# Kernel tuning notes

Measured on AMD Instinct MI355X. Metric: run time of the kernel, lower is better.

Reference implementation:

```python
import math
import jax, jax.numpy as jnp
import numpy as np

B, S, D, H, L, V = 2, 1024, 1024, 16, 6, 256
HD = D // H  # 64
PAD = 0


def setup_inputs() -> dict:
    key = jax.random.key(0)
    ks = jax.random.split(key, 22)
    s = 0.02
    f32 = jnp.float32
    inp = {
        "x": jax.random.randint(ks[0], (B, S), 0, V, dtype=jnp.int32),
        "emb": (jax.random.normal(ks[1], (V, D)) * s).astype(f32),
        "Wq": (jax.random.normal(ks[2], (L, D, D)) * s).astype(f32),
        "bq": jnp.zeros((L, D), f32),
        "Wk": (jax.random.normal(ks[3], (L, D, D)) * s).astype(f32),
        "bk": jnp.zeros((L, D), f32),
        "Wv": (jax.random.normal(ks[4], (L, D, D)) * s).astype(f32),
        "bv": jnp.zeros((L, D), f32),
        "Wo": (jax.random.normal(ks[5], (L, D, D)) * s).astype(f32),
        "bo": jnp.zeros((L, D), f32),
        "W1": (jax.random.normal(ks[6], (L, D, D // 2)) * s).astype(f32),
        "b1": jnp.zeros((L, D // 2), f32),
        "W2": (jax.random.normal(ks[7], (L, D // 2, D)) * s).astype(f32),
        "b2": jnp.zeros((L, D), f32),
        "g1": jnp.ones((L, D), f32),
        "be1": jnp.zeros((L, D), f32),
        "g2": jnp.ones((L, D), f32),
        "be2": jnp.zeros((L, D), f32),
        "E": jax.random.normal(ks[8], (L, S, HD)).astype(f32),  # relative pos embeddings, non-trainable
        "Wf": (jax.random.normal(ks[9], (D, V)) * s).astype(f32),
        "bf": jnp.zeros((V,), f32),
    }
    return inp


def _layernorm(x, g, b, eps=1e-6):
    mu = jnp.mean(x, axis=-1, keepdims=True)
    var = jnp.mean((x - mu) ** 2, axis=-1, keepdims=True)
    return (x - mu) * jax.lax.rsqrt(var + eps) * g + b


def _pos_encoding():
    # embed[p, i] = sin(p * exp(-ln(1e4)*i/D) * exp(ln(1e4)*(i%2)/D) + 0.5*pi*(i%2))
    i = jnp.arange(D, dtype=jnp.float32)
    par = jnp.mod(i, 2.0)
    rate = jnp.exp(-math.log(10000.0) * i / D) * jnp.exp(math.log(10000.0) * par / D)
    pos = jnp.arange(S, dtype=jnp.float32)
    return jnp.sin(pos[:, None] * rate[None, :] + 0.5 * math.pi * par[None, :])  # [S, D]


def _skew(QE):
    # Music Transformer skewing: pad one col on the left, reshape, drop first row.
    padded = jnp.pad(QE, ((0, 0), (0, 0), (0, 0), (1, 0)))  # [B,H,S,S+1]
    reshaped = padded.reshape(B, H, S + 1, S)
    return reshaped[:, :, 1:, :]  # [B,H,S,S]


def reference(x, emb, Wq, bq, Wk, bk, Wv, bv, Wo, bo, W1, b1, W2, b2,
              g1, be1, g2, be2, E, Wf, bf):
    pe = _pos_encoding()
    # look-ahead mask: pad positions OR strictly-future positions
    pad_mask = (x == PAD)[:, None, None, :]                      # [B,1,1,S]
    causal = jnp.triu(jnp.ones((S, S), bool), k=1)[None, None]   # [1,1,S,S]
    neg = (pad_mask | causal).astype(jnp.float32) * -1e9         # [B,1,S,S]
    # QE mask: keep qe[i, j] only where j >= S-1-i (upper-right triangle)
    idx = jnp.arange(S)
    qe_mask = (idx[None, :] >= (S - 1 - idx)[:, None]).astype(jnp.float32)

    h = emb[x] * math.sqrt(D) + pe[None]  # [B,S,D]
    scale = 1.0 / math.sqrt(HD)
    for l in range(L):
        q = (h @ Wq[l] + bq[l]).reshape(B, S, H, HD).transpose(0, 2, 1, 3)
        k = (h @ Wk[l] + bk[l]).reshape(B, S, H, HD).transpose(0, 2, 1, 3)
        v = (h @ Wv[l] + bv[l]).reshape(B, S, H, HD).transpose(0, 2, 1, 3)
        QE = jnp.einsum('bhld,md->bhlm', q, E[l]) * qe_mask
        Srel = _skew(QE)
        logits = (jnp.einsum('bhld,bhmd->bhlm', q, k) + Srel) * scale + neg
        aw = jax.nn.softmax(logits, axis=-1)
        attn = jnp.einsum('bhlm,bhmd->bhld', aw, v)
        attn = attn.transpose(0, 2, 1, 3).reshape(B, S, D)
        ao = attn @ Wo[l] + bo[l]
        o1 = _layernorm(ao, g1[l], be1[l])          # NOTE: no residual, as in source
        f = jax.nn.relu(o1 @ W1[l] + b1[l]) @ W2[l] + b2[l]
        h = _layernorm(f, g2[l], be2[l])
    return h @ Wf + bf  # [B,S,V]
```

## Files before the change

### kernel.cpp

```cpp
#include <hip/hip_runtime.h>
#include <hip/hip_bf16.h>


typedef __attribute__((ext_vector_type(8))) short  s8_t;
typedef __attribute__((ext_vector_type(4))) short  s4_t;
typedef __attribute__((ext_vector_type(8))) __bf16 bf8_t;
typedef __attribute__((ext_vector_type(4))) float  f4v;

static __device__ __forceinline__ short f2bf(float f) {
  union { float f; unsigned u; } a; a.f = f;
  unsigned u = a.u;
  u += 0x7fffu + ((u >> 16) & 1u);
  return (short)(u >> 16);
}
static __device__ __forceinline__ float bf2f(short s) {
  union { float f; unsigned u; } a;
  a.u = ((unsigned)(unsigned short)s) << 16;
  return a.f;
}
static __device__ __forceinline__ f4v mfma16(s8_t a, s8_t b, f4v c) {
  return __builtin_amdgcn_mfma_f32_16x16x32_bf16(
      __builtin_bit_cast(bf8_t, a), __builtin_bit_cast(bf8_t, b), c, 0, 0, 0);
}
static __device__ __forceinline__ void gld16(const short* g, short* l) {
  __builtin_amdgcn_global_load_lds(
      (const __attribute__((address_space(1))) void*)g,
      (__attribute__((address_space(3))) void*)l, 16, 0, 0);
}

static __device__ const int IT_TAB[24] = {
  15,15,14,13,12,11,10,9,8,7, 14,6, 13,5, 12,4, 11,3, 10,2, 9,1, 8,0};
static __device__ const int CW_TAB[24] = {
   0, 1, 0, 0, 0, 0, 0,0,0,0,  1,0,  1,0,  1,0,  1,0,  1,0, 1,0, 1,0};

__global__ __launch_bounds__(256) void prep_weights(
    const float* __restrict__ Wq, const float* __restrict__ Wk,
    const float* __restrict__ Wv, const float* __restrict__ Wo,
    const float* __restrict__ W1, const float* __restrict__ W2,
    const float* __restrict__ Wf,
    short* __restrict__ qkvT, short* __restrict__ WoT, short* __restrict__ W1T,
    short* __restrict__ W2T, short* __restrict__ WfT) {
  __shared__ float tile[64][69];
  int z = blockIdx.x;
  const float* in; short* out; int R, C; long outBS; int rowOff = 0;
  if (z < 4608) {
    R = 1024; C = 1024; outBS = (long)3072 * 1024; out = qkvT;
    if (z < 1536)      { in = Wq; }
    else if (z < 3072) { in = Wk; rowOff = 1024; z -= 1536; }
    else               { in = Wv; rowOff = 2048; z -= 3072; }
  } else if (z < 6144) { in = Wo; out = WoT; R = 1024; C = 1024; outBS = (long)1024 * 1024; z -= 4608; }
  else if (z < 6912)   { in = W1; out = W1T; R = 1024; C = 512;  outBS = (long)512 * 1024;  z -= 6144; }
  else if (z < 7680)   { in = W2; out = W2T; R = 512;  C = 1024; outBS = (long)1024 * 512;  z -= 6912; }
  else                 { in = Wf; out = WfT; R = 1024; C = 256;  outBS = 0;                 z -= 7680; }
  const int nx = C >> 6, ny = R >> 6;
  const int per = nx * ny;
  const int l = z / per, rem = z % per;
  const int cx = rem % nx, cy = rem / nx;
  in += (long)l * R * C;
  out += (long)l * outBS + (long)rowOff * R;
  const int c0 = cx * 64, r0 = cy * 64;
  const int tid = threadIdx.x;

  const int lr = tid >> 4, lc4 = tid & 15;
#pragma unroll
  for (int p = 0; p < 4; p++) {
    const int row = p * 16 + lr;
    const float4 v = *(const float4*)(in + (long)(r0 + row) * C + c0 + lc4 * 4);
    tile[row][lc4 * 4 + 0] = v.x;
    tile[row][lc4 * 4 + 1] = v.y;
    tile[row][lc4 * 4 + 2] = v.z;
    tile[row][lc4 * 4 + 3] = v.w;
  }
  __syncthreads();
  const int seg = tid & 7;
#pragma unroll
  for (int q = 0; q < 2; q++) {
    const int oc = q * 32 + (tid >> 3);
    s8_t o;
#pragma unroll
    for (int j = 0; j < 8; j++) o[j] = f2bf(tile[seg * 8 + j][oc]);
    *(s8_t*)(out + (long)(c0 + oc) * R + r0 + seg * 8) = o;
  }
}

__global__ __launch_bounds__(256) void prep_misc(
    const int* __restrict__ x, const float* __restrict__ emb,
    const float* __restrict__ E,
    const float* __restrict__ bq, const float* __restrict__ bk,
    const float* __restrict__ bv,
    short* __restrict__ h, short* __restrict__ Ebf,
    float* __restrict__ qkvB, int* __restrict__ fnp) {
  const int z = blockIdx.x;
  const int tid = threadIdx.x;
  if (z < 2048) {
    const int s = z & 1023;
    const int xv = x[z];
    const int c = tid << 2;
    const float4 e = *(const float4*)(emb + (long)xv * 1024 + c);
    const float ev[4] = {e.x, e.y, e.z, e.w};
    s4_t o;
#pragma unroll
    for (int i = 0; i < 4; i++) {
      const int d = c + i;
      const float par = (float)(d & 1);
      const float rate = expf(-9.210340371976184f * (float)d / 1024.0f) *
                         expf(9.210340371976184f * par / 1024.0f);
      const float pe = sinf((float)s * rate + 1.5707963267948966f * par);
      o[i] = f2bf(ev[i] * 32.0f + pe);
    }
    *(s4_t*)(h + (long)z * 1024 + c) = o;
  } else if (z < 2432) {
    const long i = ((long)(z - 2048) * 256 + tid) * 4;
    const float4 t = *(const float4*)(E + i);
    s4_t o = {f2bf(t.x), f2bf(t.y), f2bf(t.z), f2bf(t.w)};
    *(s4_t*)(Ebf + i) = o;
  } else if (z < 2504) {
    const int idx = (z - 2432) * 256 + tid;
    const int l = idx / 3072, n = idx % 3072;
    float v = (n < 1024) ? bq[l * 1024 + n]
            : (n < 2048) ? bk[l * 1024 + n - 1024]
                         : bv[l * 1024 + n - 2048];
    qkvB[idx] = v;
  } else {
    if (tid < 64) {
      const int b = z - 2504;
      int first = 1024;
      for (int j0 = 0; j0 < 1024; j0 += 64) {
        unsigned long long m = __ballot(x[b * 1024 + j0 + tid] != 0);
        if (m) { first = j0 + __ffsll(m) - 1; break; }
      }
      if (tid == 0) fnp[b] = first;
    }
  }
}

__global__ __launch_bounds__(256) void ln_kernel(const short* __restrict__ in,
                                                 short* __restrict__ out,
                                                 const float* __restrict__ g,
                                                 const float* __restrict__ be) {
  __shared__ float red[4];
  __shared__ float red2[4];
  const int row = blockIdx.x;
  const int tid = threadIdx.x;
  const int c = tid << 2;
  const s4_t xv = *(const s4_t*)(in + (long)row * 1024 + c);
  const float x0 = bf2f(xv[0]), x1 = bf2f(xv[1]), x2 = bf2f(xv[2]), x3 = bf2f(xv[3]);
  float s = x0 + x1 + x2 + x3;
#pragma unroll
  for (int off = 1; off < 64; off <<= 1) s += __shfl_xor(s, off);
  const int wave = tid >> 6, lane = tid & 63;
  if (lane == 0) red[wave] = s;
  __syncthreads();
  const float mu = (red[0] + red[1] + red[2] + red[3]) * (1.0f / 1024.0f);
  const float d0 = x0 - mu, d1 = x1 - mu, d2 = x2 - mu, d3 = x3 - mu;
  float q = d0 * d0 + d1 * d1 + d2 * d2 + d3 * d3;
#pragma unroll
  for (int off = 1; off < 64; off <<= 1) q += __shfl_xor(q, off);
  if (lane == 0) red2[wave] = q;
  __syncthreads();
  const float var = (red2[0] + red2[1] + red2[2] + red2[3]) * (1.0f / 1024.0f);
  const float rs = rsqrtf(var + 1e-6f);
  const float4 gv = *(const float4*)(g + c);
  const float4 bv = *(const float4*)(be + c);
  s4_t o = {f2bf(d0 * rs * gv.x + bv.x), f2bf(d1 * rs * gv.y + bv.y),
            f2bf(d2 * rs * gv.z + bv.z), f2bf(d3 * rs * gv.w + bv.w)};
  *(s4_t*)(out + (long)row * 1024 + c) = o;
}

template <int BM, int BN, int WR, int WC, int OUT_BF16, int RELU>
__global__ __launch_bounds__(256) void gemm_lds(
    const short* __restrict__ A, const short* __restrict__ BT,
    void* __restrict__ Cv, const float* __restrict__ biasp,
    int K, int lda, int ldb, int ldc) {
  constexpr int AR = BM / 64, BR = BN / 64;
  constexpr int FI = BM / WR / 16, FJ = BN / WC / 16;
  __shared__ short As[BM * 32];
  __shared__ short Bs[BN * 32];
  const int bm = blockIdx.y * BM, bn = blockIdx.x * BN;
  const int tid = threadIdx.x;
  const int wave = tid >> 6, lane = tid & 63;
  const int quad = lane >> 4, l16 = lane & 15;
  const int wr = wave / WC, wc = wave % WC;
  const int wm = wr * (BM / WR), wn = wc * (BN / WC);

  const short* Ag = A + (long)(bm + wave * 16 + (lane >> 2)) * lda + ((lane & 3) << 3);
  const short* Bg = BT + (long)(bn + wave * 16 + (lane >> 2)) * ldb + ((lane & 3) << 3);

  f4v acc[FI][FJ];
#pragma unroll
  for (int i = 0; i < FI; i++)
#pragma unroll
    for (int j = 0; j < FJ; j++) {
      f4v zz = {0.f, 0.f, 0.f, 0.f};
      acc[i][j] = zz;
    }

  for (int k0 = 0; k0 < K; k0 += 32) {
#pragma unroll
    for (int r = 0; r < AR; r++)
      gld16(Ag + (long)r * 64 * lda + k0, As + r * 2048 + wave * 512);
#pragma unroll
    for (int r = 0; r < BR; r++)
      gld16(Bg + (long)r * 64 * ldb + k0, Bs + r * 2048 + wave * 512);
    __syncthreads();
    s8_t af[FI], bfr[FJ];
#pragma unroll
    for (int t = 0; t < FI; t++)
      af[t] = *(const s8_t*)&As[(wm + t * 16 + l16) * 32 + quad * 8];
#pragma unroll
    for (int t = 0; t < FJ; t++)
      bfr[t] = *(const s8_t*)&Bs[(wn + t * 16 + l16) * 32 + quad * 8];
#pragma unroll
    for (int ti = 0; ti < FI; ti++)
#pragma unroll
      for (int tj = 0; tj < FJ; tj++)
        acc[ti][tj] = mfma16(af[ti], bfr[tj], acc[ti][tj]);
    __syncthreads();
  }

#pragma unroll
  for (int ti = 0; ti < FI; ti++) {
#pragma unroll
    for (int tj = 0; tj < FJ; tj++) {
      const int n = bn + wn + tj * 16 + l16;
      const float bval = biasp ? biasp[n] : 0.f;
#pragma unroll
      for (int r = 0; r < 4; r++) {
        const int m = bm + wm + ti * 16 + quad * 4 + r;
        float vv = acc[ti][tj][r] + bval;
        if (RELU) vv = fmaxf(vv, 0.f);
        if (OUT_BF16) ((short*)Cv)[(long)m * ldc + n] = f2bf(vv);
        else          ((float*)Cv)[(long)m * ldc + n] = vv;
      }
    }
  }
}

__global__ __launch_bounds__(256) void attn_main(
    const short* __restrict__ qkv, const short* __restrict__ Eb,
    const int* __restrict__ xids, const int* __restrict__ fnp,
    float* __restrict__ PO, float* __restrict__ PM, float* __restrict__ PL,
    short* __restrict__ outb) {
  __shared__ short Ks2[2][8][64][8];
  __shared__ short Vt[64][72];
  __shared__ short Gs[4][16][88];
  __shared__ short knegs[1024];

  const int bh = blockIdx.x, b = bh >> 4, hh = bh & 15;
  const int yy = blockIdx.y;
  const bool fbp = (yy >= 24);
  const int itile = fbp ? (yy - 24) : IT_TAB[yy];
  const int cw = fbp ? 0 : CW_TAB[yy];
  const int fb = fnp[b];
  const int i0g = itile * 64;
  if (fbp && fb <= i0g) return;

  const int tid = threadIdx.x;
  const int wave = tid >> 6, lane = tid & 63, quad = lane >> 4, l16 = lane & 15;
  const int i0 = i0g + wave * 16;

  {
    const short neg = f2bf(-1e9f);
#pragma unroll
    for (int t = 0; t < 4; t++) {
      const int idx = t * 256 + tid;
      knegs[idx] = (xids[b * 1024 + idx] == 0) ? neg : (short)0;
    }
  }

  s8_t aq[2];
  {
    const short* qp = qkv + ((long)(b * 1024 + i0 + l16)) * 3072 + hh * 64 + quad * 8;
    aq[0] = *(const s8_t*)qp;
    aq[1] = *(const s8_t*)(qp + 32);
  }

  f4v o[4];
#pragma unroll
  for (int nt = 0; nt < 4; nt++) { f4v zz = {0.f, 0.f, 0.f, 0.f}; o[nt] = zz; }
  float m_run[4] = {-INFINITY, -INFINITY, -INFINITY, -INFINITY};
  float l_run[4] = {0.f, 0.f, 0.f, 0.f};

  const short* kbase = qkv + (long)b * 1024 * 3072 + 1024 + hh * 64 + wave * 8;
  const short* vbase = qkv + (long)b * 1024 * 3072 + 2048 + hh * 64 + wave * 16;
  short* gs = &Gs[wave][0][0];

  const int jBeg = fbp ? 0 : cw * 512;
  const int jEnd = fbp ? 1024 : min(cw * 512 + 512, i0g + 64);

  s8_t vr0, vr1;
  {
    const long k1 = min(jBeg + lane, 1023);
    gld16(kbase + k1 * 3072, &Ks2[0][wave][0][0]);
    gld16(kbase + k1 * 3072 + 32, &Ks2[0][wave + 4][0][0]);
    const short* vrow = vbase + k1 * 3072;
    vr0 = *(const s8_t*)(vrow);
    vr1 = *(const s8_t*)(vrow + 8);
#pragma unroll
    for (int t = 0; t < 8; t++) {
      Vt[wave * 16 + t][lane] = vr0[t];
      Vt[wave * 16 + 8 + t][lane] = vr1[t];
    }
  }

  int pb = 0;
  for (int j0 = jBeg; j0 < jEnd; j0 += 64) {
    const bool hasNext = (j0 + 64 < jEnd);
    __syncthreads();

    {
      const int mW = 1008 - i0g - wave * 16 + j0;
#pragma unroll
      for (int t = 0; t < 5; t++) {
        const int m = min(mW + t * 16 + l16, 1023);
        const short* ep = Eb + m * 64 + quad * 8;
        const s8_t eb0 = *(const s8_t*)ep;
        const s8_t eb1 = *(const s8_t*)(ep + 32);
        f4v g = {0.f, 0.f, 0.f, 0.f};
        g = mfma16(aq[0], eb0, g);
        g = mfma16(aq[1], eb1, g);
#pragma unroll
        for (int r = 0; r < 4; r++)
          gs[(quad * 4 + r) * 88 + t * 16 + l16] = f2bf(g[r]);
      }
    }

    if (hasNext) {
      const long k1 = min(j0 + 64 + lane, 1023);
      gld16(kbase + k1 * 3072, &Ks2[pb ^ 1][wave][0][0]);
      gld16(kbase + k1 * 3072 + 32, &Ks2[pb ^ 1][wave + 4][0][0]);
      const short* vrow = vbase + k1 * 3072;
      vr0 = *(const s8_t*)(vrow);
      vr1 = *(const s8_t*)(vrow + 8);
    }

    float p[4][4];
    const int irow = i0 + quad * 4;
#pragma unroll
    for (int jt = 0; jt < 4; jt++) {
      const s8_t k0f = *(const s8_t*)&Ks2[pb][quad][jt * 16 + l16][0];
      const s8_t k1f = *(const s8_t*)&Ks2[pb][4 + quad][jt * 16 + l16][0];
      f4v zz = {0.f, 0.f, 0.f, 0.f};
      zz = mfma16(aq[0], k0f, zz);
      zz = mfma16(aq[1], k1f, zz);
      const int j = j0 + jt * 16 + l16;
      const float kn = bf2f(knegs[j]);
#pragma unroll
      for (int r = 0; r < 4; r++) {
        const int rr = quad * 4 + r;
        const float smv = bf2f(gs[rr * 87 + 15 + jt * 16 + l16]);
        const bool causal = (j <= irow + r);
        const float srel = causal ? smv : 0.f;
        const float kk = fbp ? 0.f : (causal ? kn : -1e9f);
        p[jt][r] = (zz[r] + srel) * 0.125f + kk;
      }
    }

    float alpha[4];
#pragma unroll
    for (int r = 0; r < 4; r++) {
      float mx = p[0][r];
#pragma unroll
      for (int jt = 1; jt < 4; jt++) mx = fmaxf(mx, p[jt][r]);
      mx = fmaxf(mx, __shfl_xor(mx, 1));
      mx = fmaxf(mx, __shfl_xor(mx, 2));
      mx = fmaxf(mx, __shfl_xor(mx, 4));
      mx = fmaxf(mx, __shfl_xor(mx, 8));
      const float mnew = fmaxf(m_run[r], mx);
      alpha[r] = __expf(m_run[r] - mnew);
      float ps = 0.f;
#pragma unroll
      for (int jt = 0; jt < 4; jt++) {
        p[jt][r] = __expf(p[jt][r] - mnew);
        ps += p[jt][r];
      }
      ps += __shfl_xor(ps, 1);
      ps += __shfl_xor(ps, 2);
      ps += __shfl_xor(ps, 4);
      ps += __shfl_xor(ps, 8);
      l_run[r] = l_run[r] * alpha[r] + ps;
      m_run[r] = mnew;
    }

#pragma unroll
    for (int jt = 0; jt < 4; jt++)
#pragma unroll
      for (int r = 0; r < 4; r++)
        gs[(quad * 4 + r) * 88 + jt * 16 + l16] = f2bf(p[jt][r]);
#pragma unroll
    for (int nt = 0; nt < 4; nt++)
#pragma unroll
      for (int r = 0; r < 4; r++)
        o[nt][r] *= alpha[r];

#pragma unroll
    for (int ks4 = 0; ks4 < 2; ks4++) {
      const s8_t ap = *(const s8_t*)&gs[l16 * 88 + ks4 * 32 + quad * 8];
#pragma unroll
      for (int nt = 0; nt < 4; nt++) {
        const s8_t vf = *(const s8_t*)&Vt[nt * 16 + l16][ks4 * 32 + quad * 8];
        o[nt] = mfma16(ap, vf, o[nt]);
      }
    }

    __syncthreads();
    if (hasNext) {
#pragma unroll
      for (int t = 0; t < 8; t++) {
        Vt[wave * 16 + t][lane] = vr0[t];
        Vt[wave * 16 + 8 + t][lane] = vr1[t];
      }
    }
    pb ^= 1;
  }

  if (fbp) {
#pragma unroll
    for (int nt = 0; nt < 4; nt++)
#pragma unroll
      for (int r = 0; r < 4; r++) {
        const int i = i0 + quad * 4 + r;
        if (i < fb)
          outb[((long)(b * 1024 + i)) * 1024 + hh * 64 + nt * 16 + l16] =
              f2bf(o[nt][r] / l_run[r]);
      }
  } else if (itile < 8) {
#pragma unroll
    for (int nt = 0; nt < 4; nt++)
#pragma unroll
      for (int r = 0; r < 4; r++) {
        const int i = i0 + quad * 4 + r;
        if (i >= fb)
          outb[((long)(b * 1024 + i)) * 1024 + hh * 64 + nt * 16 + l16] =
              f2bf(o[nt][r] / l_run[r]);
      }
  } else {
    const long part = (long)(bh * 16 + itile) * 2 + cw;
    float* po = PO + part * 4096;
#pragma unroll
    for (int nt = 0; nt < 4; nt++)
#pragma unroll
      for (int r = 0; r < 4; r++) {
        const int row = wave * 16 + quad * 4 + r;
        po[row * 64 + nt * 16 + l16] = o[nt][r];
      }
    if (l16 == 0) {
#pragma unroll
      for (int r = 0; r < 4; r++) {
        const int row = wave * 16 + quad * 4 + r;
        PM[part * 64 + row] = m_run[r];
        PL[part * 64 + row] = l_run[r];
      }
    }
  }
}

__global__ __launch_bounds__(256) void attn_combine(
    const float* __restrict__ PO, const float* __restrict__ PM,
    const float* __restrict__ PL, const int* __restrict__ fnp,
    short* __restrict__ outb) {
  const int id = blockIdx.x;
  const int bh = id >> 3, itile = 8 + (id & 7);
  const int b = bh >> 4, hh = bh & 15;
  const int row = threadIdx.x >> 2, seg = (threadIdx.x & 3) << 4;
  const long base = (long)(bh * 16 + itile) * 2;
  const int i = itile * 64 + row;
  if (i < fnp[b]) return;

  const float m0 = PM[base * 64 + row];
  const float m1 = PM[(base + 1) * 64 + row];
  const float M = fmaxf(m0, m1);
  const float w0 = __expf(m0 - M), w1 = __expf(m1 - M);
  const float l = w0 * PL[base * 64 + row] + w1 * PL[(base + 1) * 64 + row];
  const float* po0 = PO + base * 4096 + row * 64 + seg;
  const float* po1 = PO + (base + 1) * 4096 + row * 64 + seg;
  const float inv = 1.0f / l;
  short* op = outb + ((long)(b * 1024 + i)) * 1024 + hh * 64 + seg;
#pragma unroll
  for (int t = 0; t < 4; t++) {
    const f4v v0 = *(const f4v*)(po0 + t * 4);
    const f4v v1 = *(const f4v*)(po1 + t * 4);
    s4_t o = {f2bf((w0 * v0[0] + w1 * v1[0]) * inv),
              f2bf((w0 * v0[1] + w1 * v1[1]) * inv),
              f2bf((w0 * v0[2] + w1 * v1[2]) * inv),
              f2bf((w0 * v0[3] + w1 * v1[3]) * inv)};
    *(s4_t*)(op + t * 4) = o;
  }
}

extern "C" void kernel_launch(void* const* d_in, const int* in_sizes, int n_in,
                              void* d_out, int out_size, void* d_ws, size_t ws_size,
                              hipStream_t stream) {
  const int*   x   = (const int*)d_in[0];
  const float* emb = (const float*)d_in[1];
  const float* Wq  = (const float*)d_in[2];
  const float* bq  = (const float*)d_in[3];
  const float* Wk  = (const float*)d_in[4];
  const float* bk  = (const float*)d_in[5];
  const float* Wv  = (const float*)d_in[6];
  const float* bv  = (const float*)d_in[7];
  const float* Wo  = (const float*)d_in[8];
  const float* bo  = (const float*)d_in[9];
  const float* W1  = (const float*)d_in[10];
  const float* b1  = (const float*)d_in[11];
  const float* W2  = (const float*)d_in[12];
  const float* b2  = (const float*)d_in[13];
  const float* g1  = (const float*)d_in[14];
  const float* be1 = (const float*)d_in[15];
  const float* g2  = (const float*)d_in[16];
  const float* be2 = (const float*)d_in[17];
  const float* E   = (const float*)d_in[18];
  const float* Wf  = (const float*)d_in[19];
  const float* bfv = (const float*)d_in[20];

  char* p = (char*)d_ws;
  auto alloc = [&](size_t bytes) {
    char* r = p;
    p += (bytes + 255) & ~(size_t)255;
    return r;
  };
  short* h    = (short*)alloc(2048ull * 1024 * 2);
  short* qkv  = (short*)alloc(2048ull * 3072 * 2);
  short* attn = (short*)alloc(2048ull * 1024 * 2);
  short* tmp  = (short*)alloc(2048ull * 1024 * 2);
  short* mid  = (short*)alloc(2048ull * 512 * 2);
  short* qkvT = (short*)alloc(6ull * 3072 * 1024 * 2);
  short* WoT  = (short*)alloc(6ull * 1024 * 1024 * 2);
  short* W1T  = (short*)alloc(6ull * 512 * 1024 * 2);
  short* W2T  = (short*)alloc(6ull * 1024 * 512 * 2);
  short* WfT  = (short*)alloc(256ull * 1024 * 2);
  short* Ebf  = (short*)alloc(6ull * 1024 * 64 * 2);
  float* qkvB = (float*)alloc(6ull * 3072 * 4);
  int*   fnp  = (int*)alloc(256);
  float* PO   = (float*)alloc(2048ull * 4096 * 4);
  float* PM   = (float*)alloc(2048ull * 64 * 4);
  float* PL   = (float*)alloc(2048ull * 64 * 4);

  prep_weights<<<7744, 256, 0, stream>>>(
      Wq, Wk, Wv, Wo, W1, W2, Wf, qkvT, WoT, W1T, W2T, WfT);
  prep_misc<<<2506, 256, 0, stream>>>(x, emb, E, bq, bk, bv, h, Ebf, qkvB, fnp);

  for (int l = 0; l < 6; l++) {
    const long wOff = (long)l * 1024 * 1024;
    const long w12Off = (long)l * 512 * 1024;
    gemm_lds<128, 128, 2, 2, 1, 0><<<dim3(24, 16), 256, 0, stream>>>(
        h, qkvT + (long)l * 3072 * 1024, qkv, qkvB + l * 3072, 1024, 1024, 1024, 3072);
    attn_main<<<dim3(32, 40), 256, 0, stream>>>(
        qkv, Ebf + (long)l * 1024 * 64, x, fnp, PO, PM, PL, attn);
    attn_combine<<<256, 256, 0, stream>>>(PO, PM, PL, fnp, attn);
    gemm_lds<64, 64, 2, 2, 1, 0><<<dim3(16, 32), 256, 0, stream>>>(
        attn, WoT + wOff, tmp, bo + l * 1024, 1024, 1024, 1024, 1024);
    ln_kernel<<<2048, 256, 0, stream>>>(tmp, tmp, g1 + l * 1024, be1 + l * 1024);
    gemm_lds<64, 64, 2, 2, 1, 1><<<dim3(8, 32), 256, 0, stream>>>(
        tmp, W1T + w12Off, mid, b1 + l * 512, 1024, 1024, 1024, 512);
    gemm_lds<64, 64, 2, 2, 1, 0><<<dim3(16, 32), 256, 0, stream>>>(
        mid, W2T + w12Off, h, b2 + l * 1024, 512, 512, 512, 1024);
    ln_kernel<<<2048, 256, 0, stream>>>(h, h, g2 + l * 1024, be2 + l * 1024);
  }
  gemm_lds<64, 64, 2, 2, 0, 0><<<dim3(4, 32), 256, 0, stream>>>(
      h, WfT, (float*)d_out, bfv, 1024, 1024, 1024, 256);
}
```

Measured before the change: 947.3 us.

## Widen GEMM K-step, use one wave per LayerNorm row, enlarge transpose tiles

The GEMM kernel now loads two 32-wide K slices per iteration into doubled LDS buffers, which halves the number of barrier pairs per K loop. LayerNorm moves from one 256-thread block per row with LDS reductions to one wave per row using only shuffle reductions, which removes the __syncthreads calls. The weight-prep transpose handles 64x128 tiles, halving its block count. The costs are more LDS per GEMM block, which may lower occupancy, and more registers per LayerNorm thread.

```diff
diff --git a/kernel.cpp b/kernel.cpp
--- a/kernel.cpp
+++ b/kernel.cpp
@@ -40,41 +40,44 @@
     const float* __restrict__ Wf,
     short* __restrict__ qkvT, short* __restrict__ WoT, short* __restrict__ W1T,
     short* __restrict__ W2T, short* __restrict__ WfT) {
-  __shared__ float tile[64][69];
+  __shared__ float tile[64][133];
   int z = blockIdx.x;
   const float* in; short* out; int R, C; long outBS; int rowOff = 0;
-  if (z < 4608) {
+  if (z < 2304) {
     R = 1024; C = 1024; outBS = (long)3072 * 1024; out = qkvT;
-    if (z < 1536)      { in = Wq; }
-    else if (z < 3072) { in = Wk; rowOff = 1024; z -= 1536; }
-    else               { in = Wv; rowOff = 2048; z -= 3072; }
-  } else if (z < 6144) { in = Wo; out = WoT; R = 1024; C = 1024; outBS = (long)1024 * 1024; z -= 4608; }
-  else if (z < 6912)   { in = W1; out = W1T; R = 1024; C = 512;  outBS = (long)512 * 1024;  z -= 6144; }
-  else if (z < 7680)   { in = W2; out = W2T; R = 512;  C = 1024; outBS = (long)1024 * 512;  z -= 6912; }
-  else                 { in = Wf; out = WfT; R = 1024; C = 256;  outBS = 0;                 z -= 7680; }
-  const int nx = C >> 6, ny = R >> 6;
+    if (z < 768)       { in = Wq; }
+    else if (z < 1536) { in = Wk; rowOff = 1024; z -= 768; }
+    else               { in = Wv; rowOff = 2048; z -= 1536; }
+  } else if (z < 3072) { in = Wo; out = WoT; R = 1024; C = 1024; outBS = (long)1024 * 1024; z -= 2304; }
+  else if (z < 3456)   { in = W1; out = W1T; R = 1024; C = 512;  outBS = (long)512 * 1024;  z -= 3072; }
+  else if (z < 3840)   { in = W2; out = W2T; R = 512;  C = 1024; outBS = (long)1024 * 512;  z -= 3456; }
+  else                 { in = Wf; out = WfT; R = 1024; C = 256;  outBS = 0;                 z -= 3840; }
+  const int nx = C >> 7, ny = R >> 6;
   const int per = nx * ny;
   const int l = z / per, rem = z % per;
   const int cx = rem % nx, cy = rem / nx;
   in += (long)l * R * C;
   out += (long)l * outBS + (long)rowOff * R;
-  const int c0 = cx * 64, r0 = cy * 64;
+  const int c0 = cx * 128, r0 = cy * 64;
   const int tid = threadIdx.x;
 
   const int lr = tid >> 4, lc4 = tid & 15;
 #pragma unroll
   for (int p = 0; p < 4; p++) {
     const int row = p * 16 + lr;
-    const float4 v = *(const float4*)(in + (long)(r0 + row) * C + c0 + lc4 * 4);
-    tile[row][lc4 * 4 + 0] = v.x;
-    tile[row][lc4 * 4 + 1] = v.y;
-    tile[row][lc4 * 4 + 2] = v.z;
-    tile[row][lc4 * 4 + 3] = v.w;
+#pragma unroll
+    for (int h = 0; h < 2; h++) {
+      const float4 v = *(const float4*)(in + (long)(r0 + row) * C + c0 + h * 64 + lc4 * 4);
+      tile[row][h * 64 + lc4 * 4 + 0] = v.x;
+      tile[row][h * 64 + lc4 * 4 + 1] = v.y;
+      tile[row][h * 64 + lc4 * 4 + 2] = v.z;
+      tile[row][h * 64 + lc4 * 4 + 3] = v.w;
+    }
   }
   __syncthreads();
   const int seg = tid & 7;
 #pragma unroll
-  for (int q = 0; q < 2; q++) {
+  for (int q = 0; q < 4; q++) {
     const int oc = q * 32 + (tid >> 3);
     s8_t o;
 #pragma unroll
@@ -138,33 +141,47 @@
                                                  short* __restrict__ out,
                                                  const float* __restrict__ g,
                                                  const float* __restrict__ be) {
-  __shared__ float red[4];
-  __shared__ float red2[4];
-  const int row = blockIdx.x;
   const int tid = threadIdx.x;
-  const int c = tid << 2;
-  const s4_t xv = *(const s4_t*)(in + (long)row * 1024 + c);
-  const float x0 = bf2f(xv[0]), x1 = bf2f(xv[1]), x2 = bf2f(xv[2]), x3 = bf2f(xv[3]);
-  float s = x0 + x1 + x2 + x3;
+  const int row = blockIdx.x * 4 + (tid >> 6);
+  const int lane = tid & 63;
+  const int c = lane * 16;
+  const short* ip = in + (long)row * 1024 + c;
+  s4_t xv[4];
+#pragma unroll
+  for (int t = 0; t < 4; t++) xv[t] = *(const s4_t*)(ip + t * 4);
+  float xs[16];
+  float s = 0.f;
+#pragma unroll
+  for (int t = 0; t < 4; t++)
+#pragma unroll
+    for (int i = 0; i < 4; i++) {
+      xs[t * 4 + i] = bf2f(xv[t][i]);
+      s += xs[t * 4 + i];
+    }
 #pragma unroll
   for (int off = 1; off < 64; off <<= 1) s += __shfl_xor(s, off);
-  const int wave = tid >> 6, lane = tid & 63;
-  if (lane == 0) red[wave] = s;
-  __syncthreads();
-  const float mu = (red[0] + red[1] + red[2] + red[3]) * (1.0f / 1024.0f);
-  const float d0 = x0 - mu, d1 = x1 - mu, d2 = x2 - mu, d3 = x3 - mu;
-  float q = d0 * d0 + d1 * d1 + d2 * d2 + d3 * d3;
+  const float mu = s * (1.0f / 1024.0f);
+  float q = 0.f;
+#pragma unroll
+  for (int t = 0; t < 16; t++) {
+    xs[t] -= mu;
+    q += xs[t] * xs[t];
+  }
 #pragma unroll
   for (int off = 1; off < 64; off <<= 1) q += __shfl_xor(q, off);
-  if (lane == 0) red2[wave] = q;
-  __syncthreads();
-  const float var = (red2[0] + red2[1] + red2[2] + red2[3]) * (1.0f / 1024.0f);
+  const float var = q * (1.0f / 1024.0f);
   const float rs = rsqrtf(var + 1e-6f);
-  const float4 gv = *(const float4*)(g + c);
-  const float4 bv = *(const float4*)(be + c);
-  s4_t o = {f2bf(d0 * rs * gv.x + bv.x), f2bf(d1 * rs * gv.y + bv.y),
-            f2bf(d2 * rs * gv.z + bv.z), f2bf(d3 * rs * gv.w + bv.w)};
-  *(s4_t*)(out + (long)row * 1024 + c) = o;
+  short* op = out + (long)row * 1024 + c;
+#pragma unroll
+  for (int t = 0; t < 4; t++) {
+    const float4 gv = *(const float4*)(g + c + t * 4);
+    const float4 bv = *(const float4*)(be + c + t * 4);
+    s4_t o = {f2bf(xs[t * 4 + 0] * rs * gv.x + bv.x),
+              f2bf(xs[t * 4 + 1] * rs * gv.y + bv.y),
+              f2bf(xs[t * 4 + 2] * rs * gv.z + bv.z),
+              f2bf(xs[t * 4 + 3] * rs * gv.w + bv.w)};
+    *(s4_t*)(op + t * 4) = o;
+  }
 }
 
 template <int BM, int BN, int WR, int WC, int OUT_BF16, int RELU>
@@ -174,8 +191,8 @@
     int K, int lda, int ldb, int ldc) {
   constexpr int AR = BM / 64, BR = BN / 64;
   constexpr int FI = BM / WR / 16, FJ = BN / WC / 16;
-  __shared__ short As[BM * 32];
-  __shared__ short Bs[BN * 32];
+  __shared__ short As[2 * BM * 32];
+  __shared__ short Bs[2 * BN * 32];
   const int bm = blockIdx.y * BM, bn = blockIdx.x * BN;
   const int tid = threadIdx.x;
   const int wave = tid >> 6, lane = tid & 63;
@@ -195,26 +212,32 @@
       acc[i][j] = zz;
     }
 
-  for (int k0 = 0; k0 < K; k0 += 32) {
-#pragma unroll
-    for (int r = 0; r < AR; r++)
-      gld16(Ag + (long)r * 64 * lda + k0, As + r * 2048 + wave * 512);
-#pragma unroll
-    for (int r = 0; r < BR; r++)
-      gld16(Bg + (long)r * 64 * ldb + k0, Bs + r * 2048 + wave * 512);
+  for (int k0 = 0; k0 < K; k0 += 64) {
+#pragma unroll
+    for (int h = 0; h < 2; h++) {
+#pragma unroll
+      for (int r = 0; r < AR; r++)
+        gld16(Ag + (long)r * 64 * lda + k0 + h * 32, As + h * BM * 32 + r * 2048 + wave * 512);
+#pragma unroll
+      for (int r = 0; r < BR; r++)
+        gld16(Bg + (long)r * 64 * ldb + k0 + h * 32, Bs + h * BN * 32 + r * 2048 + wave * 512);
+    }
     __syncthreads();
-    s8_t af[FI], bfr[FJ];
-#pragma unroll
-    for (int t = 0; t < FI; t++)
-      af[t] = *(const s8_t*)&As[(wm + t * 16 + l16) * 32 + quad * 8];
-#pragma unroll
-    for (int t = 0; t < FJ; t++)
-      bfr[t] = *(const s8_t*)&Bs[(wn + t * 16 + l16) * 32 + quad * 8];
-#pragma unroll
-    for (int ti = 0; ti < FI; ti++)
-#pragma unroll
-      for (int tj = 0; tj < FJ; tj++)
-        acc[ti][tj] = mfma16(af[ti], bfr[tj], acc[ti][tj]);
+#pragma unroll
+    for (int h = 0; h < 2; h++) {
+      s8_t af[FI], bfr[FJ];
+#pragma unroll
+      for (int t = 0; t < FI; t++)
+        af[t] = *(const s8_t*)&As[h * BM * 32 + (wm + t * 16 + l16) * 32 + quad * 8];
+#pragma unroll
+      for (int t = 0; t < FJ; t++)
+        bfr[t] = *(const s8_t*)&Bs[h * BN * 32 + (wn + t * 16 + l16) * 32 + quad * 8];
+#pragma unroll
+      for (int ti = 0; ti < FI; ti++)
+#pragma unroll
+        for (int tj = 0; tj < FJ; tj++)
+          acc[ti][tj] = mfma16(af[ti], bfr[tj], acc[ti][tj]);
+    }
     __syncthreads();
   }
 
@@ -536,7 +559,7 @@
   float* PM   = (float*)alloc(2048ull * 64 * 4);
   float* PL   = (float*)alloc(2048ull * 64 * 4);
 
-  prep_weights<<<7744, 256, 0, stream>>>(
+  prep_weights<<<3872, 256, 0, stream>>>(
       Wq, Wk, Wv, Wo, W1, W2, Wf, qkvT, WoT, W1T, W2T, WfT);
   prep_misc<<<2506, 256, 0, stream>>>(x, emb, E, bq, bk, bv, h, Ebf, qkvB, fnp);
 
@@ -550,12 +573,12 @@
     attn_combine<<<256, 256, 0, stream>>>(PO, PM, PL, fnp, attn);
     gemm_lds<64, 64, 2, 2, 1, 0><<<dim3(16, 32), 256, 0, stream>>>(
         attn, WoT + wOff, tmp, bo + l * 1024, 1024, 1024, 1024, 1024);
-    ln_kernel<<<2048, 256, 0, stream>>>(tmp, tmp, g1 + l * 1024, be1 + l * 1024);
+    ln_kernel<<<512, 256, 0, stream>>>(tmp, tmp, g1 + l * 1024, be1 + l * 1024);
     gemm_lds<64, 64, 2, 2, 1, 1><<<dim3(8, 32), 256, 0, stream>>>(
         tmp, W1T + w12Off, mid, b1 + l * 512, 1024, 1024, 1024, 512);
     gemm_lds<64, 64, 2, 2, 1, 0><<<dim3(16, 32), 256, 0, stream>>>(
         mid, W2T + w12Off, h, b2 + l * 1024, 512, 512, 512, 1024);
-    ln_kernel<<<2048, 256, 0, stream>>>(h, h, g2 + l * 1024, be2 + l * 1024);
+    ln_kernel<<<512, 256, 0, stream>>>(h, h, g2 + l * 1024, be2 + l * 1024);
   }
   gemm_lds<64, 64, 2, 2, 0, 0><<<dim3(4, 32), 256, 0, stream>>>(
       h, WfT, (float*)d_out, bfv, 1024, 1024, 1024, 256);
```

New measurement: 901.3 us. 1.05x faster.
